# Optimization experiments

Hardware: AMD Instinct MI355X
Metric: run time of the kernel (lower is better)

The kernel has to match this reference:

```python
import jax, jax.numpy as jnp
import numpy as np

N = 16384
E = 524288
D_IN = 256
D_OUT = 256


def setup_inputs() -> dict:
    key = jax.random.key(0)
    k1, k2, k3, k4, k5, k6 = jax.random.split(key, 6)
    x = jax.random.normal(k1, (N, D_IN), dtype=jnp.float32)
    edge_index = jax.random.randint(k2, (2, E), 0, N, dtype=jnp.int64)
    W_update = jax.random.normal(k3, (D_OUT, D_IN), dtype=jnp.float32) / np.sqrt(D_IN)
    b_update = jax.random.normal(k4, (D_OUT,), dtype=jnp.float32) * 0.01
    W_aggregate = jax.random.normal(k5, (D_OUT, D_IN), dtype=jnp.float32) / np.sqrt(D_IN)
    b_aggregate = jax.random.normal(k6, (D_OUT,), dtype=jnp.float32) * 0.01
    return {
        "x": x,
        "edge_index": edge_index,
        "W_update": W_update,
        "b_update": b_update,
        "W_aggregate": W_aggregate,
        "b_aggregate": b_aggregate,
    }


def reference(x, edge_index, W_update, b_update, W_aggregate, b_aggregate):
    n = x.shape[0]
    src, dst = edge_index[0], edge_index[1]
    # Dense symmetric 0/1 adjacency built with SET semantics (duplicate edges
    # contribute 1, not their count) -- faithful to the torch indexing assign.
    adj = jnp.zeros((n, n), dtype=x.dtype)
    adj = adj.at[src, dst].set(1.0)
    adj = adj.at[dst, src].set(1.0)
    messages = adj @ x                                   # [N, D_in]
    aggregated = messages @ W_aggregate.T + b_aggregate  # [N, D_out]
    updated = x @ W_update.T + b_update + aggregated     # [N, D_out]
    return updated
```

## Files before the change

kernel.cpp:

```cpp
#include <hip/hip_runtime.h>
#include <hip/hip_fp16.h>

#define NN 16384
#define DD 256
#define CAP 160
#define NB 128
#define BK 64
#define LDAP 72
#define PL 2097152

typedef __attribute__((ext_vector_type(8))) __bf16 bf16x8;
typedef __attribute__((ext_vector_type(8))) unsigned short u16x8;
typedef __attribute__((ext_vector_type(4))) float f32x4;

__device__ __forceinline__ unsigned short f2bn(float f) {
    __bf16 h = (__bf16)f;
    return __builtin_bit_cast(unsigned short, h);
}

__global__ __launch_bounds__(512) void k_hist(const int* __restrict__ ei,
                                              unsigned short* __restrict__ H,
                                              const float* __restrict__ Wu,
                                              const float* __restrict__ Wa,
                                              unsigned short* __restrict__ wb,
                                              int E, int epb) {
    const int b = blockIdx.x;
    const int t = threadIdx.x;

    if (b >= NB) {
        const int w = b - NB;
        const float* src = (w < 4) ? Wu : Wa;
        unsigned short* dst = wb + ((w < 4) ? 0 : 65536);
        const int c0 = (w & 3) * 4096;
#pragma unroll
        for (int i = 0; i < 8; ++i) {
            const int f4 = c0 + i * 512 + t;
            float4 v = *(const float4*)(src + (size_t)f4 * 4);
            ushort4 o;
            o.x = f2bn(v.x); o.y = f2bn(v.y); o.z = f2bn(v.z); o.w = f2bn(v.w);
            *(ushort4*)(dst + (size_t)f4 * 4) = o;
        }
        return;
    }

    __shared__ unsigned int h[NN / 2];
    for (int i = t; i < NN / 2; i += 512) h[i] = 0u;
    __syncthreads();

    const int e0 = b * epb;
    const int e1 = min(e0 + epb, E);
    for (int e = e0 + t; e < e1; e += 512) {
        const int s = ei[e];
        const int d = ei[E + e];
        atomicAdd(&h[s >> 1], 1u << ((s & 1) << 4));
        atomicAdd(&h[d >> 1], 1u << ((d & 1) << 4));
    }
    __syncthreads();

    unsigned short* Hb = H + (size_t)b * NN;
    for (int r = t; r < NN; r += 512)
        Hb[r] = (unsigned short)((h[r >> 1] >> ((r & 1) << 4)) & 0xffffu);
}

__global__ __launch_bounds__(512) void k_gemm_scan(const float* __restrict__ x,
                                                   const unsigned short* __restrict__ wb,
                                                   const float* __restrict__ bu,
                                                   const float* __restrict__ ba,
                                                   unsigned short* __restrict__ H,
                                                   unsigned int* __restrict__ cnt,
                                                   float* __restrict__ out,
                                                   __half* __restrict__ xab) {
    __shared__ __align__(16) unsigned short As[128 * LDAP];
    __shared__ __align__(16) unsigned short Bs[256 * LDAP];

    const int t = threadIdx.x;

    if (blockIdx.x >= 256) {
        const int r = (blockIdx.x - 256) * 512 + t;
        unsigned int base = 0;
#pragma unroll 8
        for (int bb = 0; bb < NB; ++bb) {
            const size_t a = (size_t)bb * NN + r;
            const unsigned int v = H[a];
            H[a] = (unsigned short)base;
            base += v;
        }
        cnt[r] = base;
        return;
    }

    const int lane = t & 63;
    const int wid = t >> 6;
    const int wr = wid >> 2;
    const int wc = wid & 3;
    const int row0 = (blockIdx.x >> 1) << 7;
    const int colp = blockIdx.x & 1;
    const unsigned short* Wsrc = wb + ((size_t)colp << 16);

    f32x4 acc[4][4] = {};

    for (int k0 = 0; k0 < DD; k0 += BK) {
        float4 ga[4];
        uint4 rb[4];
#pragma unroll
        for (int i = 0; i < 4; ++i) {
            const int ca = i * 512 + t;
            const int ar = ca >> 4, as = ca & 15;
            ga[i] = *(const float4*)(x + (size_t)(row0 + ar) * DD + k0 + as * 4);
            const int cb = i * 512 + t;
            const int br = cb >> 3, bs = cb & 7;
            rb[i] = *(const uint4*)(Wsrc + (size_t)br * DD + k0 + bs * 8);
        }
        __syncthreads();
#pragma unroll
        for (int i = 0; i < 4; ++i) {
            const int ca = i * 512 + t;
            const int ar = ca >> 4, as = ca & 15;
            ushort4 ap;
            ap.x = f2bn(ga[i].x); ap.y = f2bn(ga[i].y);
            ap.z = f2bn(ga[i].z); ap.w = f2bn(ga[i].w);
            *(ushort4*)(&As[ar * LDAP + as * 4]) = ap;
            const int cb = i * 512 + t;
            const int br = cb >> 3, bs = cb & 7;
            *(uint4*)(&Bs[br * LDAP + bs * 8]) = rb[i];
        }
        __syncthreads();
#pragma unroll
        for (int kk = 0; kk < 2; ++kk) {
            bf16x8 av[4], bv[4];
#pragma unroll
            for (int f = 0; f < 4; ++f) {
                uint4 ra = *(const uint4*)(&As[(wr * 64 + f * 16 + (lane & 15)) * LDAP + kk * 32 + (lane >> 4) * 8]);
                av[f] = __builtin_bit_cast(bf16x8, ra);
                uint4 rv = *(const uint4*)(&Bs[(wc * 64 + f * 16 + (lane & 15)) * LDAP + kk * 32 + (lane >> 4) * 8]);
                bv[f] = __builtin_bit_cast(bf16x8, rv);
            }
#pragma unroll
            for (int fm = 0; fm < 4; ++fm)
#pragma unroll
                for (int fn = 0; fn < 4; ++fn)
                    acc[fm][fn] = __builtin_amdgcn_mfma_f32_16x16x32_bf16(
                        av[fm], bv[fn], acc[fm][fn], 0, 0, 0);
        }
    }

    const int gr0 = row0 + wr * 64 + ((lane >> 4) << 2);
    const int gc0 = wc * 64 + (lane & 15);
    if (colp == 0) {
#pragma unroll
        for (int fn = 0; fn < 4; ++fn) {
            const int c = gc0 + fn * 16;
            const float bias = bu[c] + ba[c];
#pragma unroll
            for (int fm = 0; fm < 4; ++fm) {
                const int r = gr0 + fm * 16;
#pragma unroll
                for (int i = 0; i < 4; ++i)
                    out[(size_t)(r + i) * DD + c] = acc[fm][fn][i] + bias;
            }
        }
    } else {
#pragma unroll
        for (int fn = 0; fn < 4; ++fn) {
            const int c = gc0 + fn * 16;
            const size_t pbase = (size_t)(c >> 7) * PL + (c & 127);
#pragma unroll
            for (int fm = 0; fm < 4; ++fm) {
                const int r = gr0 + fm * 16;
#pragma unroll
                for (int i = 0; i < 4; ++i)
                    xab[pbase + (size_t)(r + i) * 128] = __float2half(acc[fm][fn][i]);
            }
        }
    }
}

__global__ __launch_bounds__(512) void k_fill(const int* __restrict__ ei,
                                              const unsigned short* __restrict__ H,
                                              unsigned short* __restrict__ list,
                                              int E, int epb) {
    __shared__ unsigned int off[NN / 2];
    const int b = blockIdx.x;
    const int t = threadIdx.x;
    for (int i = t; i < NN / 2; i += 512) off[i] = 0u;
    __syncthreads();

    const unsigned short* Hb = H + (size_t)b * NN;
    const int e0 = b * epb;
    const int e1 = min(e0 + epb, E);
    for (int e = e0 + t; e < e1; e += 512) {
        const int s = ei[e];
        const int d = ei[E + e];
        const int sh1 = (s & 1) << 4;
        const unsigned int o1 = atomicAdd(&off[s >> 1], 1u << sh1);
        const int p1 = (int)Hb[s] + (int)((o1 >> sh1) & 0xffffu);
        if (p1 < CAP) list[(size_t)s * CAP + p1] = (unsigned short)d;
        const int sh2 = (d & 1) << 4;
        const unsigned int o2 = atomicAdd(&off[d >> 1], 1u << sh2);
        const int p2 = (int)Hb[d] + (int)((o2 >> sh2) & 0xffffu);
        if (p2 < CAP) list[(size_t)d * CAP + p2] = (unsigned short)s;
    }
}

#define ACC4(S, V) { \
    acc[S][0] = __hadd2(acc[S][0], __builtin_bit_cast(__half2, (V).x)); \
    acc[S][1] = __hadd2(acc[S][1], __builtin_bit_cast(__half2, (V).y)); \
    acc[S][2] = __hadd2(acc[S][2], __builtin_bit_cast(__half2, (V).z)); \
    acc[S][3] = __hadd2(acc[S][3], __builtin_bit_cast(__half2, (V).w)); }

__device__ __forceinline__ void gather_plane(const unsigned short* lst, int n,
                                             const __half* __restrict__ plane,
                                             float* __restrict__ out,
                                             int row, int outoff, int lane) {
    const int lg = lane >> 4;
    const int li = lane & 15;
    __half2 acc[4][4];
    const __half2 z2 = __float2half2_rn(0.0f);
#pragma unroll
    for (int s = 0; s < 4; ++s) { acc[s][0] = z2; acc[s][1] = z2; acc[s][2] = z2; acc[s][3] = z2; }

    int i = 0;
    for (; i + 32 <= n; i += 32) {
        const u16x8 e = *(const u16x8*)(lst + i + lg * 8);
        uint4 v[8];
#pragma unroll
        for (int j = 0; j < 8; ++j)
            v[j] = *(const uint4*)(plane + ((size_t)e[j] << 7) + li * 8);
#pragma unroll
        for (int j = 0; j < 8; ++j) ACC4(j & 3, v[j]);
    }
    for (; i + 4 <= n; i += 4) {
        uint4 v = *(const uint4*)(plane + ((size_t)lst[i + lg] << 7) + li * 8);
        ACC4(0, v);
    }
    if (i < n && lg < n - i) {
        uint4 v = *(const uint4*)(plane + ((size_t)lst[i + lg] << 7) + li * 8);
        ACC4(1, v);
    }

#pragma unroll
    for (int k = 0; k < 4; ++k) {
        acc[0][k] = __hadd2(acc[0][k], __hadd2(acc[1][k], __hadd2(acc[2][k], acc[3][k])));
        int v = __builtin_bit_cast(int, acc[0][k]);
        v = __shfl_xor(v, 16, 64);
        acc[0][k] = __hadd2(acc[0][k], __builtin_bit_cast(__half2, v));
        v = __builtin_bit_cast(int, acc[0][k]);
        v = __shfl_xor(v, 32, 64);
        acc[0][k] = __hadd2(acc[0][k], __builtin_bit_cast(__half2, v));
    }

    if (lg == 0) {
        float4* po = (float4*)(out + (size_t)row * DD + outoff + li * 8);
        float4 o0 = po[0], o1 = po[1];
        float2 f;
        f = __half22float2(acc[0][0]); o0.x += f.x; o0.y += f.y;
        f = __half22float2(acc[0][1]); o0.z += f.x; o0.w += f.y;
        f = __half22float2(acc[0][2]); o1.x += f.x; o1.y += f.y;
        f = __half22float2(acc[0][3]); o1.z += f.x; o1.w += f.y;
        po[0] = o0; po[1] = o1;
    }
}

__global__ __launch_bounds__(256) void k_gatherA(const unsigned int* __restrict__ cnt,
                                                 const unsigned short* __restrict__ list,
                                                 unsigned short* __restrict__ nlist,
                                                 unsigned int* __restrict__ ncnt,
                                                 const __half* __restrict__ xab,
                                                 float* __restrict__ out) {
    __shared__ uint4 bmv[4][128];
    __shared__ unsigned short lst[4][CAP];

    const int t = threadIdx.x;
    const int wid = t >> 6;
    const int lane = t & 63;
    const int row = (blockIdx.x << 2) + wid;

    uint4 z; z.x = 0u; z.y = 0u; z.z = 0u; z.w = 0u;
    bmv[wid][lane] = z;
    bmv[wid][64 + lane] = z;
    const int m = min((int)cnt[row], CAP);
    __syncthreads();

    unsigned int* bw = (unsigned int*)&bmv[wid][0];
    const unsigned short* gl = list + (size_t)row * CAP;
    for (int i = lane; i < m; i += 64) {
        const int idx = gl[i];
        atomicOr(&bw[idx >> 5], 1u << (idx & 31));
    }
    __syncthreads();

    int base = 0;
#pragma unroll
    for (int g = 0; g < 2; ++g) {
        const int q = (g << 6) + lane;
        uint4 w = bmv[wid][q];
        int c = __popc(w.x) + __popc(w.y) + __popc(w.z) + __popc(w.w);
        int incl = c;
#pragma unroll
        for (int dd = 1; dd < 64; dd <<= 1) {
            int y = __shfl_up(incl, dd, 64);
            if (lane >= dd) incl += y;
        }
        int pos = base + incl - c;
        const int wbase = q << 7;
        unsigned int bb; int bit;
        bb = w.x; while (bb) { bit = __ffs(bb) - 1; bb &= bb - 1;
            if (pos < CAP) lst[wid][pos] = (unsigned short)(wbase + bit); ++pos; }
        bb = w.y; while (bb) { bit = __ffs(bb) - 1; bb &= bb - 1;
            if (pos < CAP) lst[wid][pos] = (unsigned short)(wbase + 32 + bit); ++pos; }
        bb = w.z; while (bb) { bit = __ffs(bb) - 1; bb &= bb - 1;
            if (pos < CAP) lst[wid][pos] = (unsigned short)(wbase + 64 + bit); ++pos; }
        bb = w.w; while (bb) { bit = __ffs(bb) - 1; bb &= bb - 1;
            if (pos < CAP) lst[wid][pos] = (unsigned short)(wbase + 96 + bit); ++pos; }
        base += __shfl(incl, 63, 64);
    }
    __syncthreads();

    const int n = min(base, CAP);
    if (lane == 0) ncnt[row] = (unsigned int)n;
    for (int i = lane; i < n; i += 64) nlist[(size_t)row * CAP + i] = lst[wid][i];

    gather_plane(lst[wid], n, xab, out, row, 0, lane);
}

__global__ __launch_bounds__(256) void k_gatherB(const unsigned int* __restrict__ ncnt,
                                                 const unsigned short* __restrict__ nlist,
                                                 const __half* __restrict__ xab,
                                                 float* __restrict__ out) {
    __shared__ unsigned short lst[4][CAP];

    const int t = threadIdx.x;
    const int wid = t >> 6;
    const int lane = t & 63;
    const int row = (blockIdx.x << 2) + wid;

    const int n = min((int)ncnt[row], CAP);
    const unsigned short* gl = nlist + (size_t)row * CAP;
    for (int i = lane; i < n; i += 64) lst[wid][i] = gl[i];
    __syncthreads();

    gather_plane(lst[wid], n, xab + PL, out, row, 128, lane);
}

extern "C" void kernel_launch(void* const* d_in, const int* in_sizes, int n_in,
                              void* d_out, int out_size, void* d_ws, size_t ws_size,
                              hipStream_t stream) {
    const float* x  = (const float*)d_in[0];
    const int*   ei = (const int*)d_in[1];
    const float* Wu = (const float*)d_in[2];
    const float* bu = (const float*)d_in[3];
    const float* Wa = (const float*)d_in[4];
    const float* ba = (const float*)d_in[5];
    float* out = (float*)d_out;

    const int E = in_sizes[1] / 2;
    const int epb = (E + NB - 1) / NB;

    char* ws = (char*)d_ws;
    __half* xab = (__half*)ws;
    unsigned short* wb = (unsigned short*)(ws + 8388608);
    unsigned short* H = (unsigned short*)(ws + 9437184);
    unsigned int* cnt = (unsigned int*)(ws + 13631488);
    unsigned short* list = (unsigned short*)(ws + 14680064);
    unsigned short* nlist = (unsigned short*)(ws + 19922944);
    unsigned int* ncnt = (unsigned int*)(ws + 25165824);

    k_hist<<<NB + 8, 512, 0, stream>>>(ei, H, Wu, Wa, wb, E, epb);
    k_gemm_scan<<<288, 512, 0, stream>>>(x, wb, bu, ba, H, cnt, out, xab);
    k_fill<<<NB, 512, 0, stream>>>(ei, H, list, E, epb);
    k_gatherA<<<NN / 4, 256, 0, stream>>>(cnt, list, nlist, ncnt, xab, out);
    k_gatherB<<<NN / 4, 256, 0, stream>>>(ncnt, nlist, xab, out);
}
```

Before: 93.69 us.

## Replace bitmap-scan dedup with zero-row redirect and pre-convert x to bf16

Duplicate neighbours are now detected with atomicOr in the gather kernel itself and redirected to an appended zero row. This replaces the bitmap popcount/prefix-scan compaction and drops the nlist/ncnt intermediate, so both gather passes share one kernel that reads the raw edge list. x is converted to bf16 in a prep kernel, so the GEMM loads half the bytes and skips in-loop conversion. The cost is an extra full pass over x, dedup work done twice (once per plane), and gathers that still load the wasted zero-row entries.

```diff
diff --git a/kernel.cpp b/kernel.cpp
--- a/kernel.cpp
+++ b/kernel.cpp
@@ -7,7 +7,7 @@
 #define NB 128
 #define BK 64
 #define LDAP 72
-#define PL 2097152
+#define PLP 2099200
 
 typedef __attribute__((ext_vector_type(8))) __bf16 bf16x8;
 typedef __attribute__((ext_vector_type(8))) unsigned short u16x8;
@@ -18,27 +18,45 @@
     return __builtin_bit_cast(unsigned short, h);
 }
 
-__global__ __launch_bounds__(512) void k_hist(const int* __restrict__ ei,
+__global__ __launch_bounds__(512) void k_prep(const int* __restrict__ ei,
                                               unsigned short* __restrict__ H,
+                                              const float* __restrict__ x,
                                               const float* __restrict__ Wu,
                                               const float* __restrict__ Wa,
+                                              unsigned short* __restrict__ xb,
                                               unsigned short* __restrict__ wb,
+                                              __half* __restrict__ xab,
                                               int E, int epb) {
     const int b = blockIdx.x;
     const int t = threadIdx.x;
 
-    if (b >= NB) {
-        const int w = b - NB;
-        const float* src = (w < 4) ? Wu : Wa;
-        unsigned short* dst = wb + ((w < 4) ? 0 : 65536);
-        const int c0 = (w & 3) * 4096;
-#pragma unroll
-        for (int i = 0; i < 8; ++i) {
-            const int f4 = c0 + i * 512 + t;
-            float4 v = *(const float4*)(src + (size_t)f4 * 4);
-            ushort4 o;
-            o.x = f2bn(v.x); o.y = f2bn(v.y); o.z = f2bn(v.z); o.w = f2bn(v.w);
-            *(ushort4*)(dst + (size_t)f4 * 4) = o;
+    if (b >= 128) {
+        if (b < 192) {
+            const int w = b - 128;
+#pragma unroll
+            for (int i = 0; i < 32; ++i) {
+                const int f4 = w * 16384 + i * 512 + t;
+                float4 v = *(const float4*)(x + (size_t)f4 * 4);
+                ushort4 o;
+                o.x = f2bn(v.x); o.y = f2bn(v.y); o.z = f2bn(v.z); o.w = f2bn(v.w);
+                *(ushort4*)(xb + (size_t)f4 * 4) = o;
+            }
+        } else if (b < 200) {
+            const int w = b - 192;
+            const float* src = (w < 4) ? Wu : Wa;
+            unsigned short* dst = wb + ((w < 4) ? 0 : 65536);
+            const int c0 = (w & 3) * 4096;
+#pragma unroll
+            for (int i = 0; i < 8; ++i) {
+                const int f4 = c0 + i * 512 + t;
+                float4 v = *(const float4*)(src + (size_t)f4 * 4);
+                ushort4 o;
+                o.x = f2bn(v.x); o.y = f2bn(v.y); o.z = f2bn(v.z); o.w = f2bn(v.w);
+                *(ushort4*)(dst + (size_t)f4 * 4) = o;
+            }
+        } else {
+            uint4 z; z.x = 0u; z.y = 0u; z.z = 0u; z.w = 0u;
+            ((uint4*)xab)[(size_t)(t >> 8) * (PLP / 8) + (NN * 128 / 8) + (t & 255)] = z;
         }
         return;
     }
@@ -62,7 +80,7 @@
         Hb[r] = (unsigned short)((h[r >> 1] >> ((r & 1) << 4)) & 0xffffu);
 }
 
-__global__ __launch_bounds__(512) void k_gemm_scan(const float* __restrict__ x,
+__global__ __launch_bounds__(512) void k_gemm_scan(const unsigned short* __restrict__ xb,
                                                    const unsigned short* __restrict__ wb,
                                                    const float* __restrict__ bu,
                                                    const float* __restrict__ ba,
@@ -100,29 +118,31 @@
     f32x4 acc[4][4] = {};
 
     for (int k0 = 0; k0 < DD; k0 += BK) {
-        float4 ga[4];
-        uint4 rb[4];
+        uint4 ra_[2], rb_[4];
+#pragma unroll
+        for (int i = 0; i < 2; ++i) {
+            const int f = i * 512 + t;
+            const int r = f >> 3, s = f & 7;
+            ra_[i] = *(const uint4*)(xb + (size_t)(row0 + r) * DD + k0 + s * 8);
+        }
 #pragma unroll
         for (int i = 0; i < 4; ++i) {
-            const int ca = i * 512 + t;
-            const int ar = ca >> 4, as = ca & 15;
-            ga[i] = *(const float4*)(x + (size_t)(row0 + ar) * DD + k0 + as * 4);
-            const int cb = i * 512 + t;
-            const int br = cb >> 3, bs = cb & 7;
-            rb[i] = *(const uint4*)(Wsrc + (size_t)br * DD + k0 + bs * 8);
+            const int f = i * 512 + t;
+            const int r = f >> 3, s = f & 7;
+            rb_[i] = *(const uint4*)(Wsrc + (size_t)r * DD + k0 + s * 8);
         }
         __syncthreads();
 #pragma unroll
+        for (int i = 0; i < 2; ++i) {
+            const int f = i * 512 + t;
+            const int r = f >> 3, s = f & 7;
+            *(uint4*)(&As[r * LDAP + s * 8]) = ra_[i];
+        }
+#pragma unroll
         for (int i = 0; i < 4; ++i) {
-            const int ca = i * 512 + t;
-            const int ar = ca >> 4, as = ca & 15;
-            ushort4 ap;
-            ap.x = f2bn(ga[i].x); ap.y = f2bn(ga[i].y);
-            ap.z = f2bn(ga[i].z); ap.w = f2bn(ga[i].w);
-            *(ushort4*)(&As[ar * LDAP + as * 4]) = ap;
-            const int cb = i * 512 + t;
-            const int br = cb >> 3, bs = cb & 7;
-            *(uint4*)(&Bs[br * LDAP + bs * 8]) = rb[i];
+            const int f = i * 512 + t;
+            const int r = f >> 3, s = f & 7;
+            *(uint4*)(&Bs[r * LDAP + s * 8]) = rb_[i];
         }
         __syncthreads();
 #pragma unroll
@@ -163,7 +183,7 @@
 #pragma unroll
         for (int fn = 0; fn < 4; ++fn) {
             const int c = gc0 + fn * 16;
-            const size_t pbase = (size_t)(c >> 7) * PL + (c & 127);
+            const size_t pbase = (size_t)(c >> 7) * PLP + (c & 127);
 #pragma unroll
             for (int fm = 0; fm < 4; ++fm) {
                 const int r = gr0 + fm * 16;
@@ -208,10 +228,33 @@
     acc[S][2] = __hadd2(acc[S][2], __builtin_bit_cast(__half2, (V).z)); \
     acc[S][3] = __hadd2(acc[S][3], __builtin_bit_cast(__half2, (V).w)); }
 
-__device__ __forceinline__ void gather_plane(const unsigned short* lst, int n,
-                                             const __half* __restrict__ plane,
-                                             float* __restrict__ out,
-                                             int row, int outoff, int lane) {
+__global__ __launch_bounds__(256) void k_gather(const unsigned int* __restrict__ cnt,
+                                                const unsigned short* __restrict__ list,
+                                                const __half* __restrict__ plane,
+                                                float* __restrict__ out,
+                                                int outoff) {
+    __shared__ unsigned int bmw[4][512];
+    __shared__ unsigned short lst[4][CAP];
+
+    const int t = threadIdx.x;
+    const int wid = t >> 6;
+    const int lane = t & 63;
+    const int row = (blockIdx.x << 2) + wid;
+
+    uint4 z4; z4.x = 0u; z4.y = 0u; z4.z = 0u; z4.w = 0u;
+    ((uint4*)&bmw[wid][0])[lane] = z4;
+    ((uint4*)&bmw[wid][0])[64 + lane] = z4;
+
+    const int m = min((int)cnt[row], CAP);
+    const unsigned short* gl = list + (size_t)row * CAP;
+    for (int i = lane; i < m; i += 64) {
+        int idx = gl[i];
+        const unsigned int bit = 1u << (idx & 31);
+        const unsigned int old = atomicOr(&bmw[wid][idx >> 5], bit);
+        if (old & bit) idx = NN;
+        lst[wid][i] = (unsigned short)idx;
+    }
+
     const int lg = lane >> 4;
     const int li = lane & 15;
     __half2 acc[4][4];
@@ -220,8 +263,8 @@
     for (int s = 0; s < 4; ++s) { acc[s][0] = z2; acc[s][1] = z2; acc[s][2] = z2; acc[s][3] = z2; }
 
     int i = 0;
-    for (; i + 32 <= n; i += 32) {
-        const u16x8 e = *(const u16x8*)(lst + i + lg * 8);
+    for (; i + 32 <= m; i += 32) {
+        const u16x8 e = *(const u16x8*)(&lst[wid][i + lg * 8]);
         uint4 v[8];
 #pragma unroll
         for (int j = 0; j < 8; ++j)
@@ -229,12 +272,12 @@
 #pragma unroll
         for (int j = 0; j < 8; ++j) ACC4(j & 3, v[j]);
     }
-    for (; i + 4 <= n; i += 4) {
-        uint4 v = *(const uint4*)(plane + ((size_t)lst[i + lg] << 7) + li * 8);
+    for (; i + 4 <= m; i += 4) {
+        uint4 v = *(const uint4*)(plane + ((size_t)lst[wid][i + lg] << 7) + li * 8);
         ACC4(0, v);
     }
-    if (i < n && lg < n - i) {
-        uint4 v = *(const uint4*)(plane + ((size_t)lst[i + lg] << 7) + li * 8);
+    if (i < m && lg < m - i) {
+        uint4 v = *(const uint4*)(plane + ((size_t)lst[wid][i + lg] << 7) + li * 8);
         ACC4(1, v);
     }
 
@@ -259,87 +302,6 @@
         f = __half22float2(acc[0][3]); o1.z += f.x; o1.w += f.y;
         po[0] = o0; po[1] = o1;
     }
-}
-
-__global__ __launch_bounds__(256) void k_gatherA(const unsigned int* __restrict__ cnt,
-                                                 const unsigned short* __restrict__ list,
-                                                 unsigned short* __restrict__ nlist,
-                                                 unsigned int* __restrict__ ncnt,
-                                                 const __half* __restrict__ xab,
-                                                 float* __restrict__ out) {
-    __shared__ uint4 bmv[4][128];
-    __shared__ unsigned short lst[4][CAP];
-
-    const int t = threadIdx.x;
-    const int wid = t >> 6;
-    const int lane = t & 63;
-    const int row = (blockIdx.x << 2) + wid;
-
-    uint4 z; z.x = 0u; z.y = 0u; z.z = 0u; z.w = 0u;
-    bmv[wid][lane] = z;
-    bmv[wid][64 + lane] = z;
-    const int m = min((int)cnt[row], CAP);
-    __syncthreads();
-
-    unsigned int* bw = (unsigned int*)&bmv[wid][0];
-    const unsigned short* gl = list + (size_t)row * CAP;
-    for (int i = lane; i < m; i += 64) {
-        const int idx = gl[i];
-        atomicOr(&bw[idx >> 5], 1u << (idx & 31));
-    }
-    __syncthreads();
-
-    int base = 0;
-#pragma unroll
-    for (int g = 0; g < 2; ++g) {
-        const int q = (g << 6) + lane;
-        uint4 w = bmv[wid][q];
-        int c = __popc(w.x) + __popc(w.y) + __popc(w.z) + __popc(w.w);
-        int incl = c;
-#pragma unroll
-        for (int dd = 1; dd < 64; dd <<= 1) {
-            int y = __shfl_up(incl, dd, 64);
-            if (lane >= dd) incl += y;
-        }
-        int pos = base + incl - c;
-        const int wbase = q << 7;
-        unsigned int bb; int bit;
-        bb = w.x; while (bb) { bit = __ffs(bb) - 1; bb &= bb - 1;
-            if (pos < CAP) lst[wid][pos] = (unsigned short)(wbase + bit); ++pos; }
-        bb = w.y; while (bb) { bit = __ffs(bb) - 1; bb &= bb - 1;
-            if (pos < CAP) lst[wid][pos] = (unsigned short)(wbase + 32 + bit); ++pos; }
-        bb = w.z; while (bb) { bit = __ffs(bb) - 1; bb &= bb - 1;
-            if (pos < CAP) lst[wid][pos] = (unsigned short)(wbase + 64 + bit); ++pos; }
-        bb = w.w; while (bb) { bit = __ffs(bb) - 1; bb &= bb - 1;
-            if (pos < CAP) lst[wid][pos] = (unsigned short)(wbase + 96 + bit); ++pos; }
-        base += __shfl(incl, 63, 64);
-    }
-    __syncthreads();
-
-    const int n = min(base, CAP);
-    if (lane == 0) ncnt[row] = (unsigned int)n;
-    for (int i = lane; i < n; i += 64) nlist[(size_t)row * CAP + i] = lst[wid][i];
-
-    gather_plane(lst[wid], n, xab, out, row, 0, lane);
-}
-
-__global__ __launch_bounds__(256) void k_gatherB(const unsigned int* __restrict__ ncnt,
-                                                 const unsigned short* __restrict__ nlist,
-                                                 const __half* __restrict__ xab,
-                                                 float* __restrict__ out) {
-    __shared__ unsigned short lst[4][CAP];
-
-    const int t = threadIdx.x;
-    const int wid = t >> 6;
-    const int lane = t & 63;
-    const int row = (blockIdx.x << 2) + wid;
-
-    const int n = min((int)ncnt[row], CAP);
-    const unsigned short* gl = nlist + (size_t)row * CAP;
-    for (int i = lane; i < n; i += 64) lst[wid][i] = gl[i];
-    __syncthreads();
-
-    gather_plane(lst[wid], n, xab + PL, out, row, 128, lane);
 }
 
 extern "C" void kernel_launch(void* const* d_in, const int* in_sizes, int n_in,
@@ -358,16 +320,15 @@
 
     char* ws = (char*)d_ws;
     __half* xab = (__half*)ws;
-    unsigned short* wb = (unsigned short*)(ws + 8388608);
-    unsigned short* H = (unsigned short*)(ws + 9437184);
-    unsigned int* cnt = (unsigned int*)(ws + 13631488);
-    unsigned short* list = (unsigned short*)(ws + 14680064);
-    unsigned short* nlist = (unsigned short*)(ws + 19922944);
-    unsigned int* ncnt = (unsigned int*)(ws + 25165824);
-
-    k_hist<<<NB + 8, 512, 0, stream>>>(ei, H, Wu, Wa, wb, E, epb);
-    k_gemm_scan<<<288, 512, 0, stream>>>(x, wb, bu, ba, H, cnt, out, xab);
+    unsigned short* wb = (unsigned short*)(ws + 8396800);
+    unsigned short* xb = (unsigned short*)(ws + 8658944);
+    unsigned short* H = (unsigned short*)(ws + 17047552);
+    unsigned int* cnt = (unsigned int*)(ws + 21241856);
+    unsigned short* list = (unsigned short*)(ws + 21307392);
+
+    k_prep<<<201, 512, 0, stream>>>(ei, H, x, Wu, Wa, xb, wb, xab, E, epb);
+    k_gemm_scan<<<288, 512, 0, stream>>>(xb, wb, bu, ba, H, cnt, out, xab);
     k_fill<<<NB, 512, 0, stream>>>(ei, H, list, E, epb);
-    k_gatherA<<<NN / 4, 256, 0, stream>>>(cnt, list, nlist, ncnt, xab, out);
-    k_gatherB<<<NN / 4, 256, 0, stream>>>(ncnt, nlist, xab, out);
-}
+    k_gather<<<NN / 4, 256, 0, stream>>>(cnt, list, xab, out, 0);
+    k_gather<<<NN / 4, 256, 0, stream>>>(cnt, list, xab + PLP, out, 128);
+}
```

Measured after the change: 112.8 us. +20.4%, slower.
